# Performance work log

Measured on AMD Instinct MI355X. Metric: run time of the kernel, lower is better.

The kernel has to match this reference:

```python
import jax, jax.numpy as jnp
import numpy as np

N = 100000   # nodes
E = 1000000  # edges
IN = 100     # input feature dim
H = 4        # heads
D = 32       # hidden per head (H*D = 128)
C = 47       # classes
EPS = 1e-5
SLOPE = 0.2  # DGL GATv2 leaky_relu negative slope


def setup_inputs() -> dict:
    key = jax.random.key(0)
    ks = jax.random.split(key, 32)
    lin = lambda k, i, o: (jax.random.normal(k, (i, o), jnp.float32) / np.float32(np.sqrt(i)))
    inp = {}
    inp['x'] = jax.random.normal(ks[0], (N, IN), jnp.float32)
    inp['src'] = jax.random.randint(ks[1], (E,), 0, N, jnp.int32)
    inp['dst'] = jnp.sort(jax.random.randint(ks[2], (E,), 0, N, jnp.int32))
    # layer 0: IN -> H*D, Linear residual (IN != H*D)
    inp['Wsrc0'] = lin(ks[3], IN, H * D); inp['bsrc0'] = jnp.zeros(H * D, jnp.float32)
    inp['Wdst0'] = lin(ks[4], IN, H * D); inp['bdst0'] = jnp.zeros(H * D, jnp.float32)
    inp['attn0'] = lin(ks[5], H, D)
    inp['Wres0'] = lin(ks[6], IN, H * D); inp['bres0'] = jnp.zeros(H * D, jnp.float32)
    # layer 1: H*D -> H*D, Identity residual (128 == 128)
    inp['Wsrc1'] = lin(ks[7], H * D, H * D); inp['bsrc1'] = jnp.zeros(H * D, jnp.float32)
    inp['Wdst1'] = lin(ks[8], H * D, H * D); inp['bdst1'] = jnp.zeros(H * D, jnp.float32)
    inp['attn1'] = lin(ks[9], H, D)
    # layer 2: H*D -> H*C, Linear residual (128 != 188)
    inp['Wsrc2'] = lin(ks[10], H * D, H * C); inp['bsrc2'] = jnp.zeros(H * C, jnp.float32)
    inp['Wdst2'] = lin(ks[11], H * D, H * C); inp['bdst2'] = jnp.zeros(H * C, jnp.float32)
    inp['attn2'] = lin(ks[12], H, C)
    inp['Wres2'] = lin(ks[13], H * D, H * C); inp['bres2'] = jnp.zeros(H * C, jnp.float32)
    # BatchNorm1d params (training-mode batch stats)
    inp['g0'] = jnp.ones(H * D, jnp.float32); inp['be0'] = jnp.zeros(H * D, jnp.float32)
    inp['g1'] = jnp.ones(H * D, jnp.float32); inp['be1'] = jnp.zeros(H * D, jnp.float32)
    return inp


def _gatv2(h, src, dst, Ws, bs, Wd, bd, attn, resval):
    """One GATv2Conv on a full block (src feats == dst feats == h)."""
    Hh, Dd = attn.shape
    fs = (h @ Ws + bs).reshape(-1, Hh, Dd)   # [N,H,D] src projection
    fd = (h @ Wd + bd).reshape(-1, Hh, Dd)   # [N,H,D] dst projection
    e = jax.nn.leaky_relu(fs[src] + fd[dst], SLOPE)         # [E,H,D]
    logits = jnp.einsum('ehd,hd->eh', e, attn)              # [E,H]
    m = jax.ops.segment_max(logits, dst, num_segments=N)    # per-dst max
    ex = jnp.exp(logits - m[dst])
    s = jax.ops.segment_sum(ex, dst, num_segments=N)
    alpha = ex / s[dst]                                      # edge softmax
    out = jax.ops.segment_sum(alpha[:, :, None] * fs[src], dst, num_segments=N)
    return out + resval                                      # [N,H,D]


def _bn(x, g, b):
    mu = x.mean(0)
    v = x.var(0)  # biased, as torch BN training mode
    return g * (x - mu) / jnp.sqrt(v + EPS) + b


def reference(x, src, dst,
              Wsrc0, bsrc0, Wdst0, bdst0, attn0, Wres0, bres0,
              Wsrc1, bsrc1, Wdst1, bdst1, attn1,
              Wsrc2, bsrc2, Wdst2, bdst2, attn2, Wres2, bres2,
              g0, be0, g1, be1):
    # layer 0: conv(+relu activation) -> flatten -> BN -> relu (dropout = eval identity)
    res0 = (x @ Wres0 + bres0).reshape(N, H, D)
    h = jax.nn.relu(_gatv2(x, src, dst, Wsrc0, bsrc0, Wdst0, bdst0, attn0, res0))
    h = jax.nn.relu(_bn(h.reshape(N, H * D), g0, be0))
    # layer 1: Identity residual
    res1 = h.reshape(N, H, D)
    h = jax.nn.relu(_gatv2(h, src, dst, Wsrc1, bsrc1, Wdst1, bdst1, attn1, res1))
    h = jax.nn.relu(_bn(h.reshape(N, H * D), g1, be1))
    # layer 2: no activation; mean over heads; log_softmax
    res2 = (h @ Wres2 + bres2).reshape(N, H, C)
    h = _gatv2(h, src, dst, Wsrc2, bsrc2, Wdst2, bdst2, attn2, res2)
    h = h.mean(1)                                # [N,C]
    return jax.nn.log_softmax(h, axis=-1)
```

## Files before the change

### kernel.cpp

```cpp
#include <hip/hip_runtime.h>
#include <hip/hip_bf16.h>

#define Nn 100000
#define Ee 1000000
#define INF_ 100
#define Hh 4
#define Dd 32
#define HD 128
#define Cc 47
#define HC 188
#define HCP 192
#define EPSV 1e-5f
#define SLOPE 0.2f
#define NBLK ((Nn + 255) / 256)

typedef __hip_bfloat16 bf16;
typedef __attribute__((ext_vector_type(8))) short short8;
typedef __attribute__((ext_vector_type(4))) float f32x4;
typedef __attribute__((ext_vector_type(2))) float f32x2;

__device__ __forceinline__ float tof(bf16 v) { return __bfloat162float(v); }
__device__ __forceinline__ float b2f(unsigned short u) {
    return __uint_as_float((unsigned)u << 16);
}
__device__ __forceinline__ float ldb(const bf16* p) {
    return b2f(*(const unsigned short*)p);
}
__device__ __forceinline__ unsigned short f2u(float v) {
    bf16 t = __float2bfloat16(v);
    return *(unsigned short*)&t;
}
__device__ __forceinline__ f32x2 pk2(float x, float y) {
    f32x2 r; r.x = x; r.y = y; return r;
}
__device__ __forceinline__ f32x2 pabs2(f32x2 v) {
    return __builtin_elementwise_max(v, -v);
}
__device__ __forceinline__ f32x2 pfma2(f32x2 a, f32x2 b, f32x2 c) {
    return __builtin_elementwise_fma(a, b, c);
}

template <int C>
__device__ __forceinline__ float dppadd(float v) {
    int m = __builtin_amdgcn_update_dpp(0, __float_as_int(v), C, 0xF, 0xF, false);
    return v + __int_as_float(m);
}
template <int C>
__device__ __forceinline__ float dppmax(float v) {
    int m = __builtin_amdgcn_update_dpp(0, __float_as_int(v), C, 0xF, 0xF, false);
    return fmaxf(v, __int_as_float(m));
}
__device__ __forceinline__ float sum16(float p) {
    p = dppadd<0xB1>(p);
    p = dppadd<0x4E>(p);
    p = dppadd<0x124>(p);
    p = dppadd<0x128>(p);
    return p;
}
__device__ __forceinline__ float max16(float p) {
    p = dppmax<0xB1>(p); p = dppmax<0x4E>(p);
    p = dppmax<0x124>(p); p = dppmax<0x128>(p);
    return p;
}

#define L2E 1.4426950408889634f
#define LN2 0.6931471805599453f

__device__ __forceinline__ float ld_any(const void* p, int i, int isbf) {
    return isbf ? tof(((const bf16*)p)[i]) : ((const float*)p)[i];
}

__device__ __forceinline__ int lbound(const int* __restrict__ dst, int n) {
    int lo = 0, hi = Ee;
    while (lo < hi) {
        int mid = (lo + hi) >> 1;
        if (dst[mid] < n) lo = mid + 1; else hi = mid;
    }
    return lo;
}

#define WROWS 1280
#define NSP 15
struct PrepTab { const void* src[8]; int row0[8]; int K[8]; int M[8]; int MP[8]; };
struct CvtTab { const void* src[NSP]; int off[NSP + 1]; };

__global__ __launch_bounds__(256) void prepare(
    const void* __restrict__ x, const int* __restrict__ src,
    const int* __restrict__ dst,
    PrepTab pt, CvtTab ct, int tot,
    bf16* __restrict__ xb, bf16* __restrict__ wtb, bf16* __restrict__ pb,
    unsigned* __restrict__ w384, unsigned* __restrict__ w256,
    int* __restrict__ ptr, int* __restrict__ cnt,
    float* __restrict__ z0, float* __restrict__ z1, int* __restrict__ flag) {
    __shared__ int wc[4];
    __shared__ int lbv[257];
    __shared__ int lh[256];
    const int t = threadIdx.x;
    unsigned w = ((const unsigned*)x)[t];
    float dv = __uint_as_float((w & 0xFFFFu) << 16);
    float da = fabsf(dv);
    unsigned long long m = __ballot(da > 1e-4f && da < 10.f);
    if ((t & 63) == 0) wc[t >> 6] = __popcll(m);
    __syncthreads();
    const int isbf = (wc[0] + wc[1] + wc[2] + wc[3]) >= 128;
    if (blockIdx.x == 0 && t == 0) *flag = isbf;

    const int gi = blockIdx.x * 256 + t;
    if (gi < Nn * 128) {
        int row = gi >> 7, col = gi & 127;
        float v = (col < INF_) ? ld_any(x, row * INF_ + col, isbf) : 0.f;
        xb[gi] = __float2bfloat16(v);
    }
    if (gi < WROWS * 128) {
        int row = gi >> 7, k = gi & 127;
        float v = 0.f;
#pragma unroll
        for (int q = 0; q < 8; ++q) {
            if (row >= pt.row0[q] && row < pt.row0[q] + pt.MP[q]) {
                int mm = row - pt.row0[q];
                if (mm < pt.M[q] && k < pt.K[q])
                    v = ld_any(pt.src[q], k * pt.M[q] + mm, isbf);
            }
        }
        wtb[gi] = __float2bfloat16(v);
    }
    if (gi < tot) {
        int seg = 0;
        while (gi >= ct.off[seg + 1]) seg++;
        pb[gi] = __float2bfloat16(ld_any(ct.src[seg], gi - ct.off[seg], isbf));
    }
    if (gi < Ee) {
        unsigned s = (unsigned)src[gi];
        w384[gi] = s * 384u;
        w256[gi] = s << 8;
    }
    if (gi < 2 * HD) { z0[gi] = 0.f; z1[gi] = 0.f; }
    if (blockIdx.x < NBLK) {
        int nn = gi;
        int lb = Ee;
        if (nn <= Nn) { lb = lbound(dst, nn); ptr[nn] = lb; }
        lbv[t] = lb;
        if (t == 255) lbv[256] = (nn + 1 <= Nn) ? lbound(dst, nn + 1) : Ee;
        lh[t] = 0;
        __syncthreads();
        if (nn < Nn) {
            int dg = lbv[t + 1] - lbv[t]; if (dg > 255) dg = 255;
            atomicAdd(&lh[dg], 1);
        }
        __syncthreads();
        cnt[t * NBLK + blockIdx.x] = lh[t];
    }
}

__global__ void deg_totals(const int* __restrict__ cnt, int* __restrict__ totals) {
    int wave = threadIdx.x >> 6, lane = threadIdx.x & 63;
    int bin = blockIdx.x * 4 + wave;
    int s = 0;
    for (int k = lane; k < NBLK; k += 64) s += cnt[bin * NBLK + k];
#pragma unroll
    for (int o = 1; o < 64; o <<= 1) s += __shfl_xor(s, o);
    if (lane == 0) totals[bin] = s;
}

__global__ void deg_bases(const int* __restrict__ cnt, const int* __restrict__ totals,
                          int* __restrict__ base) {
    int wave = threadIdx.x >> 6, lane = threadIdx.x & 63;
    int bin = blockIdx.x * 4 + wave;
    int bb = 0;
    for (int b = bin + 1 + lane; b < 256; b += 64) bb += totals[b];
#pragma unroll
    for (int o = 1; o < 64; o <<= 1) bb += __shfl_xor(bb, o);
    int run = bb;
    for (int k0 = 0; k0 < NBLK; k0 += 64) {
        int k = k0 + lane;
        int c = (k < NBLK) ? cnt[bin * NBLK + k] : 0;
        int p = c;
#pragma unroll
        for (int o = 1; o < 64; o <<= 1) {
            int t = __shfl_up(p, o);
            if (lane >= o) p += t;
        }
        if (k < NBLK) base[bin * NBLK + k] = run + (p - c);
        run += __shfl(p, 63);
    }
}

__global__ void deg_scatter_blk(const int* __restrict__ ptr, const int* __restrict__ base,
                                int* __restrict__ perm) {
    __shared__ int lh[256];
    int t = threadIdx.x;
    lh[t] = 0;
    __syncthreads();
    int n = blockIdx.x * 256 + t;
    if (n < Nn) {
        int dg = ptr[n + 1] - ptr[n]; if (dg > 255) dg = 255;
        int loc = atomicAdd(&lh[dg], 1);
        perm[base[dg * NBLK + blockIdx.x] + loc] = n;
    }
}

template <int MP, int NOUT, int CS, bool ABN, bool PAD47, int OSTR>
__global__ __launch_bounds__(256, 4) void gemm_big(
    const bf16* __restrict__ A, const bf16* __restrict__ Wt,
    const bf16* __restrict__ b0, const bf16* __restrict__ b1,
    const bf16* __restrict__ b2,
    bf16* __restrict__ o0, bf16* __restrict__ o1, bf16* __restrict__ o2,
    int MR, const float* __restrict__ sums,
    const bf16* __restrict__ gg, const bf16* __restrict__ bbn) {
    constexpr int CS64 = CS * 64;
    constexpr int PITCH = CS64 + 8;
    constexpr int LSZ = (64 * PITCH > 64 * 136) ? 64 * PITCH : 64 * 136;
    __shared__ __align__(16) bf16 Al[LSZ];
    __shared__ float scb[ABN ? HD : 1], ofb[ABN ? HD : 1];
    const int row0 = blockIdx.x * 64;
    const int tid = threadIdx.x;
    if (ABN) {
        if (tid < HD) {
            float mu = sums[tid] * (1.f / Nn);
            float var = sums[HD + tid] * (1.f / Nn) - mu * mu;
            float sc = tof(gg[tid]) * rsqrtf(var + EPSV);
            scb[tid] = sc;
            ofb[tid] = tof(bbn[tid]) - mu * sc;
        }
        __syncthreads();
    }
#pragma unroll
    for (int j = 0; j < 4; ++j) {
        int idx = tid + j * 256;
        int r = idx >> 4, kk = (idx & 15) * 8;
        int4 val = {0, 0, 0, 0};
        if (row0 + r < Nn) {
            val = *(const int4*)&A[(size_t)(row0 + r) * 128 + kk];
            if (ABN) {
                short8 av = *(short8*)&val;
                bf16 tmp[8];
#pragma unroll
                for (int u = 0; u < 8; ++u) {
                    float v = b2f((unsigned short)av[u]);
                    v = fmaxf(fmaf(v, scb[kk + u], ofb[kk + u]), 0.f);
                    tmp[u] = __float2bfloat16(v);
                }
                val = *(int4*)tmp;
            }
        }
        *(int4*)&Al[r * 136 + kk] = val;
    }
    __syncthreads();
    const int wave = tid >> 6, lane = tid & 63;
    const int n16 = lane & 15, quad = lane >> 4;
    const int colbase = blockIdx.y * CS64 + wave * (16 * CS);
    f32x4 acc[4][CS];
#pragma unroll
    for (int rt = 0; rt < 4; ++rt)
#pragma unroll
        for (int c = 0; c < CS; ++c) acc[rt][c] = (f32x4){0.f, 0.f, 0.f, 0.f};
    const bf16* wb[CS];
#pragma unroll
    for (int c = 0; c < CS; ++c)
        wb[c] = Wt + (size_t)(colbase + c * 16 + n16) * 128 + quad * 8;
    const bf16* ap = Al + n16 * 136 + quad * 8;
#pragma unroll
    for (int ks = 0; ks < 4; ++ks) {
        short8 bf[CS];
#pragma unroll
        for (int c = 0; c < CS; ++c) bf[c] = *(const short8*)(wb[c] + ks * 32);
#pragma unroll
        for (int rt = 0; rt < 4; ++rt) {
            short8 af = *(const short8*)(ap + rt * 16 * 136 + ks * 32);
#pragma unroll
            for (int c = 0; c < CS; ++c)
                acc[rt][c] = __builtin_amdgcn_mfma_f32_16x16x32_bf16(af, bf[c], acc[rt][c], 0, 0, 0);
        }
    }
    __syncthreads();
    if (PAD47) {
        for (int z = tid; z < 64 * PITCH; z += 256) Al[z] = __float2bfloat16(0.f);
        __syncthreads();
    }
#pragma unroll
    for (int c = 0; c < CS; ++c) {
        int pos = wave * (16 * CS) + c * 16 + n16;
        int col = colbase + c * 16 + n16;
        int oi = col / MP, lc = col - oi * MP;
        bool valid = (oi < NOUT) && (lc < MR);
        float bb = 0.f;
        if (valid) {
            const bf16* bp = (oi == 0) ? b0 : (oi == 1) ? b1 : b2;
            bb = tof(bp[lc]);
        }
        int stp = PAD47 ? (lc + lc / 47) : pos;
#pragma unroll
        for (int rt = 0; rt < 4; ++rt) {
#pragma unroll
            for (int i = 0; i < 4; ++i) {
                int rl = rt * 16 + quad * 4 + i;
                if (valid) Al[rl * PITCH + stp] = __float2bfloat16(acc[rt][c][i] + bb);
            }
        }
    }
    __syncthreads();
    constexpr int NG = CS64 / 8;
    for (int t = tid; t < 64 * NG; t += 256) {
        int rl = t / NG, g = t % NG;
        int row = row0 + rl;
        if (row >= Nn) continue;
        int pos0 = g * 8;
        int oi, lc0;
        if (PAD47) { oi = blockIdx.y; lc0 = pos0; }
        else {
            int col0 = blockIdx.y * CS64 + pos0;
            oi = col0 / MP; lc0 = col0 - oi * MP;
        }
        if (oi >= NOUT) continue;
        bf16* o = (oi == 0) ? o0 : (oi == 1) ? o1 : o2;
        int4 v = *(int4*)&Al[rl * PITCH + pos0];
        *(int4*)&o[(size_t)row * OSTR + lc0] = v;
    }
}

template <bool RESBN>
__global__ __launch_bounds__(256) void gat_fused_128(
    const bf16* __restrict__ fs, const bf16* __restrict__ fd,
    const unsigned* __restrict__ srcW, const int* __restrict__ ptr,
    const int* __restrict__ perm,
    const bf16* __restrict__ attn, const bf16* __restrict__ resb,
    const float* __restrict__ sums, const bf16* __restrict__ gv,
    const bf16* __restrict__ bev, bf16* __restrict__ hout) {
    const int wave = threadIdx.x >> 6, lane = threadIdx.x & 63;
    const int di = blockIdx.x * 4 + wave;
    if (di >= Nn) return;
    const int d = perm[di];
    const int c0 = lane * 2;
    const unsigned c0b = (unsigned)c0 * 2u;
    ushort2 aq = *(const ushort2*)&attn[c0];
    float a0 = b2f(aq.x) * L2E, a1 = b2f(aq.y) * L2E;
    const f32x2 Av = pk2(0.6f * a0, 0.6f * a1);
    const f32x2 Bv = pk2(0.4f * a0, 0.4f * a1);
    ushort2 dq = *(const ushort2*)&fd[(size_t)d * HD + c0];
    const f32x2 fdv = pk2(b2f(dq.x), b2f(dq.y));
    const char* fsb = (const char*)fs;
    float l = 0.f;
    f32x2 Ov = pk2(0.f, 0.f);
    int e = ptr[d];
    const int e1 = ptr[d + 1];
    for (; e < e1 && (e & 3); ++e) {
        unsigned v = srcW[e] + c0b;
        ushort2 fq = *(const ushort2*)(fsb + v);
        f32x2 f = pk2(b2f(fq.x), b2f(fq.y));
        f32x2 x = f + fdv;
        f32x2 t = pfma2(pabs2(x), Bv, x * Av);
        float p = sum16(t.x + t.y);
        float pe = __builtin_amdgcn_exp2f(p);
        l += pe;
        Ov = pfma2(pk2(pe, pe), f, Ov);
    }
    for (; e + 3 < e1; e += 4) {
        uint4 sw = *(const uint4*)&srcW[e];
        unsigned vA = sw.x + c0b, vB = sw.y + c0b;
        unsigned vC = sw.z + c0b, vD = sw.w + c0b;
        ushort2 qA = *(const ushort2*)(fsb + vA);
        ushort2 qB = *(const ushort2*)(fsb + vB);
        ushort2 qC = *(const ushort2*)(fsb + vC);
        ushort2 qD = *(const ushort2*)(fsb + vD);
        f32x2 fA = pk2(b2f(qA.x), b2f(qA.y));
        f32x2 fB = pk2(b2f(qB.x), b2f(qB.y));
        f32x2 fC = pk2(b2f(qC.x), b2f(qC.y));
        f32x2 fD = pk2(b2f(qD.x), b2f(qD.y));
        f32x2 xA = fA + fdv, xB = fB + fdv, xC = fC + fdv, xD = fD + fdv;
        f32x2 tA = pfma2(pabs2(xA), Bv, xA * Av);
        f32x2 tB = pfma2(pabs2(xB), Bv, xB * Av);
        f32x2 tC = pfma2(pabs2(xC), Bv, xC * Av);
        f32x2 tD = pfma2(pabs2(xD), Bv, xD * Av);
        float pA = tA.x + tA.y, pB = tB.x + tB.y;
        float pC = tC.x + tC.y, pD = tD.x + tD.y;
        pA = sum16(pA); pB = sum16(pB); pC = sum16(pC); pD = sum16(pD);
        float eA = __builtin_amdgcn_exp2f(pA), eB = __builtin_amdgcn_exp2f(pB);
        float eC = __builtin_amdgcn_exp2f(pC), eD = __builtin_amdgcn_exp2f(pD);
        l += (eA + eB) + (eC + eD);
        Ov = pfma2(pk2(eA, eA), fA, Ov);
        Ov = pfma2(pk2(eB, eB), fB, Ov);
        Ov = pfma2(pk2(eC, eC), fC, Ov);
        Ov = pfma2(pk2(eD, eD), fD, Ov);
    }
    for (; e < e1; ++e) {
        unsigned v = srcW[e] + c0b;
        ushort2 fq = *(const ushort2*)(fsb + v);
        f32x2 f = pk2(b2f(fq.x), b2f(fq.y));
        f32x2 x = f + fdv;
        f32x2 t = pfma2(pabs2(x), Bv, x * Av);
        float p = sum16(t.x + t.y);
        float pe = __builtin_amdgcn_exp2f(p);
        l += pe;
        Ov = pfma2(pk2(pe, pe), f, Ov);
    }
    float inv = l > 0.f ? 1.f / l : 0.f;
    ushort2 rq = *(const ushort2*)&resb[(size_t)d * HD + c0];
    float r0 = b2f(rq.x), r1 = b2f(rq.y);
    if (RESBN) {
        float mu0 = sums[c0] * (1.f / Nn), mu1 = sums[c0 + 1] * (1.f / Nn);
        float va0 = sums[HD + c0] * (1.f / Nn) - mu0 * mu0;
        float va1 = sums[HD + c0 + 1] * (1.f / Nn) - mu1 * mu1;
        float sc0 = tof(gv[c0]) * rsqrtf(va0 + EPSV);
        float sc1 = tof(gv[c0 + 1]) * rsqrtf(va1 + EPSV);
        float of0 = tof(bev[c0]) - mu0 * sc0;
        float of1 = tof(bev[c0 + 1]) - mu1 * sc1;
        r0 = fmaxf(fmaf(r0, sc0, of0), 0.f);
        r1 = fmaxf(fmaf(r1, sc1, of1), 0.f);
    }
    float v0 = fmaxf(fmaf(Ov.x, inv, r0), 0.f);
    float v1 = fmaxf(fmaf(Ov.y, inv, r1), 0.f);
    ushort2 ov; ov.x = f2u(v0); ov.y = f2u(v1);
    *(ushort2*)&hout[(size_t)d * HD + c0] = ov;
}

__global__ __launch_bounds__(256) void gat_fused_188(
    const bf16* __restrict__ fs, const bf16* __restrict__ fd,
    const unsigned* __restrict__ srcW, const int* __restrict__ ptr,
    const int* __restrict__ perm,
    const bf16* __restrict__ attn, const bf16* __restrict__ rs,
    void* __restrict__ out, const int* __restrict__ flag) {
    const int wave = threadIdx.x >> 6, lane = threadIdx.x & 63;
    const int di = blockIdx.x * 4 + wave;
    if (di >= Nn) return;
    const int d = perm[di];
    const int h = lane >> 4, j = lane & 15;
    const int c0 = h * 48 + j;
    const unsigned c0b = (unsigned)c0 * 2u;
    const int ca = h * Cc + j;
    const bool has2 = (j < 15);
    float a0 = ldb(&attn[ca]) * L2E;
    float a1 = ldb(&attn[ca + 16]) * L2E;
    float a2 = has2 ? ldb(&attn[ca + 32]) * L2E : 0.f;
    float A0 = 0.6f * a0, B0 = 0.4f * a0;
    float A1 = 0.6f * a1, B1 = 0.4f * a1;
    float A2 = 0.6f * a2, B2 = 0.4f * a2;
    const bf16* fdr = fd + (size_t)d * HCP;
    float fd0 = ldb(&fdr[c0]);
    float fd1 = ldb(&fdr[c0 + 16]);
    float fd2 = ldb(&fdr[c0 + 32]);
    const char* fsb = (const char*)fs;
    float l = 0.f, O0 = 0.f, O1 = 0.f, O2 = 0.f;
    int e = ptr[d];
    const int e1 = ptr[d + 1];
    for (; e + 3 < e1; e += 4) {
        unsigned vA = srcW[e] + c0b, vB = srcW[e + 1] + c0b;
        unsigned vC = srcW[e + 2] + c0b, vD = srcW[e + 3] + c0b;
        float fA0 = b2f(*(const unsigned short*)(fsb + vA));
        float fA1 = b2f(*(const unsigned short*)(fsb + vA + 32));
        float fA2 = b2f(*(const unsigned short*)(fsb + vA + 64));
        float fB0 = b2f(*(const unsigned short*)(fsb + vB));
        float fB1 = b2f(*(const unsigned short*)(fsb + vB + 32));
        float fB2 = b2f(*(const unsigned short*)(fsb + vB + 64));
        float fC0 = b2f(*(const unsigned short*)(fsb + vC));
        float fC1 = b2f(*(const unsigned short*)(fsb + vC + 32));
        float fC2 = b2f(*(const unsigned short*)(fsb + vC + 64));
        float fD0 = b2f(*(const unsigned short*)(fsb + vD));
        float fD1 = b2f(*(const unsigned short*)(fsb + vD + 32));
        float fD2 = b2f(*(const unsigned short*)(fsb + vD + 64));
        float xA0 = fA0 + fd0, xA1 = fA1 + fd1, xA2 = fA2 + fd2;
        float xB0 = fB0 + fd0, xB1 = fB1 + fd1, xB2 = fB2 + fd2;
        float xC0 = fC0 + fd0, xC1 = fC1 + fd1, xC2 = fC2 + fd2;
        float xD0 = fD0 + fd0, xD1 = fD1 + fd1, xD2 = fD2 + fd2;
        float pA = fmaf(xA0, A0, fmaf(fabsf(xA0), B0, fmaf(xA1, A1, fmaf(fabsf(xA1), B1,
                   fmaf(xA2, A2, fabsf(xA2) * B2)))));
        float pB = fmaf(xB0, A0, fmaf(fabsf(xB0), B0, fmaf(xB1, A1, fmaf(fabsf(xB1), B1,
                   fmaf(xB2, A2, fabsf(xB2) * B2)))));
        float pC = fmaf(xC0, A0, fmaf(fabsf(xC0), B0, fmaf(xC1, A1, fmaf(fabsf(xC1), B1,
                   fmaf(xC2, A2, fabsf(xC2) * B2)))));
        float pD = fmaf(xD0, A0, fmaf(fabsf(xD0), B0, fmaf(xD1, A1, fmaf(fabsf(xD1), B1,
                   fmaf(xD2, A2, fabsf(xD2) * B2)))));
        pA = sum16(pA); pB = sum16(pB); pC = sum16(pC); pD = sum16(pD);
        float eA = __builtin_amdgcn_exp2f(pA), eB = __builtin_amdgcn_exp2f(pB);
        float eC = __builtin_amdgcn_exp2f(pC), eD = __builtin_amdgcn_exp2f(pD);
        l += (eA + eB) + (eC + eD);
        O0 = fmaf(eA, fA0, O0); O0 = fmaf(eB, fB0, O0);
        O0 = fmaf(eC, fC0, O0); O0 = fmaf(eD, fD0, O0);
        O1 = fmaf(eA, fA1, O1); O1 = fmaf(eB, fB1, O1);
        O1 = fmaf(eC, fC1, O1); O1 = fmaf(eD, fD1, O1);
        O2 = fmaf(eA, fA2, O2); O2 = fmaf(eB, fB2, O2);
        O2 = fmaf(eC, fC2, O2); O2 = fmaf(eD, fD2, O2);
    }
    for (; e < e1; ++e) {
        unsigned v = srcW[e] + c0b;
        float f0 = b2f(*(const unsigned short*)(fsb + v));
        float f1 = b2f(*(const unsigned short*)(fsb + v + 32));
        float f2 = b2f(*(const unsigned short*)(fsb + v + 64));
        float x0 = f0 + fd0, x1 = f1 + fd1, x2 = f2 + fd2;
        float p = fmaf(x0, A0, fmaf(fabsf(x0), B0, fmaf(x1, A1, fmaf(fabsf(x1), B1,
                  fmaf(x2, A2, fabsf(x2) * B2)))));
        p = sum16(p);
        float pe = __builtin_amdgcn_exp2f(p);
        l += pe;
        O0 = fmaf(pe, f0, O0);
        O1 = fmaf(pe, f1, O1);
        O2 = fmaf(pe, f2, O2);
    }
    float inv = l > 0.f ? 1.f / l : 0.f;
    const bf16* rr = rs + (size_t)d * HCP;
    float v0 = fmaf(O0, inv, ldb(&rr[c0]));
    float v1 = fmaf(O1, inv, ldb(&rr[c0 + 16]));
    float v2 = has2 ? fmaf(O2, inv, ldb(&rr[c0 + 32])) : 0.f;
    v0 += __shfl_xor(v0, 16); v0 += __shfl_xor(v0, 32); v0 *= 0.25f;
    v1 += __shfl_xor(v1, 16); v1 += __shfl_xor(v1, 32); v1 *= 0.25f;
    v2 += __shfl_xor(v2, 16); v2 += __shfl_xor(v2, 32); v2 *= 0.25f;
    float mx = fmaxf(v0, v1);
    if (has2) mx = fmaxf(mx, v2);
    mx = max16(mx);
    float sm = __expf(v0 - mx) + __expf(v1 - mx) + (has2 ? __expf(v2 - mx) : 0.f);
    sm = sum16(sm);
    if (h == 0) {
        float ls = mx + __log2f(sm) * LN2;
        if (*flag) {
            bf16* o = (bf16*)out + (size_t)d * Cc;
            o[j] = __float2bfloat16(v0 - ls);
            o[j + 16] = __float2bfloat16(v1 - ls);
            if (has2) o[j + 32] = __float2bfloat16(v2 - ls);
        } else {
            float* o = (float*)out + (size_t)d * Cc;
            o[j] = v0 - ls;
            o[j + 16] = v1 - ls;
            if (has2) o[j + 32] = v2 - ls;
        }
    }
}

__global__ void col_stats(const bf16* __restrict__ in, float* __restrict__ sums) {
    int c = threadIdx.x;
    int r0 = blockIdx.x * 256;
    int r1 = r0 + 256; if (r1 > Nn) r1 = Nn;
    float s = 0.f, s2 = 0.f;
    for (int r = r0; r < r1; ++r) {
        float v = ldb(&in[(size_t)r * HD + c]);
        s += v; s2 += v * v;
    }
    atomicAdd(&sums[c], s);
    atomicAdd(&sums[HD + c], s2);
}

extern "C" void kernel_launch(void* const* d_in, const int* in_sizes, int n_in,
                              void* d_out, int out_size, void* d_ws, size_t ws_size,
                              hipStream_t stream) {
    (void)in_sizes; (void)n_in; (void)out_size; (void)ws_size;
    const void* x = d_in[0];
    const int* src = (const int*)d_in[1];
    const int* dst = (const int*)d_in[2];

    char* ws = (char*)d_ws;
    size_t off = 0;
    auto alloc = [&](size_t bytes) {
        void* p = ws + off;
        off += (bytes + 255) & ~(size_t)255;
        return p;
    };
    bf16* xb = (bf16*)alloc((size_t)Nn * 128 * 2);
    bf16* rb = (bf16*)alloc((size_t)Nn * HD * 2);
    bf16* rs = xb;
    bf16* fs = (bf16*)alloc((size_t)Nn * HCP * 2);
    bf16* fd = (bf16*)alloc((size_t)Nn * HCP * 2);
    bf16* hbA = (bf16*)alloc((size_t)Nn * HD * 2);
    bf16* hbB = (bf16*)alloc((size_t)Nn * HD * 2);
    int* ptr = (int*)alloc((Nn + 1) * 4);
    bf16* wtb = (bf16*)alloc((size_t)WROWS * 128 * 2);
    float* bns0 = (float*)alloc(2 * HD * 4);
    float* bns1 = (float*)alloc(2 * HD * 4);
    bf16* pb = (bf16*)alloc(4096 * 2);
    int* flag = (int*)alloc(256);
    unsigned* w384 = (unsigned*)alloc((size_t)Ee * 4);
    unsigned* w256 = (unsigned*)alloc((size_t)Ee * 4);
    int* cnt = (int*)alloc((size_t)256 * NBLK * 4);
    int* cbase = (int*)alloc((size_t)256 * NBLK * 4);
    int* totals = (int*)alloc(256 * 4);
    int* perm = (int*)alloc((size_t)Nn * 4);

    static const int spIdx[NSP] = {4, 6, 7, 9, 11, 13, 14, 16, 18, 19, 21, 22, 23, 24, 25};
    static const int spSz[NSP]  = {HD, HD, HD, HD, HD, HD, HD, HC, HC, HC, HC, HD, HD, HD, HD};
    CvtTab tab;
    int tot = 0;
    for (int i = 0; i < NSP; ++i) { tab.src[i] = d_in[spIdx[i]]; tab.off[i] = tot; tot += spSz[i]; }
    tab.off[NSP] = tot;
    const bf16 *bsrc0 = pb + tab.off[0], *bdst0 = pb + tab.off[1], *attn0 = pb + tab.off[2],
               *bres0 = pb + tab.off[3], *bsrc1 = pb + tab.off[4], *bdst1 = pb + tab.off[5],
               *attn1 = pb + tab.off[6], *bsrc2 = pb + tab.off[7], *bdst2 = pb + tab.off[8],
               *attn2 = pb + tab.off[9], *bres2 = pb + tab.off[10],
               *g0 = pb + tab.off[11], *be0 = pb + tab.off[12],
               *g1 = pb + tab.off[13], *be1 = pb + tab.off[14];

    PrepTab pt;
    static const int wIdx[8] = {3, 5, 8, 10, 12, 15, 17, 20};
    static const int wK[8]   = {INF_, INF_, INF_, HD, HD, HD, HD, HD};
    static const int wM[8]   = {HD, HD, HD, HD, HD, HC, HC, HC};
    static const int wMP[8]  = {128, 128, 128, 128, 128, 192, 192, 192};
    static const int wR0[8]  = {0, 128, 256, 384, 512, 640, 832, 1024};
    for (int i = 0; i < 8; ++i) {
        pt.src[i] = d_in[wIdx[i]]; pt.row0[i] = wR0[i];
        pt.K[i] = wK[i]; pt.M[i] = wM[i]; pt.MP[i] = wMP[i];
    }

    const int prepGrid = (Nn * 128 + 255) / 256;
    prepare<<<prepGrid, 256, 0, stream>>>(x, src, dst, pt, tab, tot,
                                          xb, wtb, pb, w384, w256, ptr, cnt,
                                          bns0, bns1, flag);
    deg_totals<<<64, 256, 0, stream>>>(cnt, totals);
    deg_bases<<<64, 256, 0, stream>>>(cnt, totals, cbase);
    deg_scatter_blk<<<NBLK, 256, 0, stream>>>(ptr, cbase, perm);

    const int fusedGrid = (Nn + 3) / 4;
    const int statsGrid = NBLK;
    const int rowBlk = (Nn + 63) / 64;

    gemm_big<128, 3, 3, false, false, HD><<<dim3(rowBlk, 2), 256, 0, stream>>>(
        xb, wtb, bsrc0, bdst0, bres0, fs, fd, rb, HD, nullptr, nullptr, nullptr);
    gat_fused_128<false><<<fusedGrid, 256, 0, stream>>>(fs, fd, w256, ptr, perm,
                                                        attn0, rb, nullptr, nullptr,
                                                        nullptr, hbA);
    col_stats<<<statsGrid, 128, 0, stream>>>(hbA, bns0);

    gemm_big<128, 2, 2, true, false, HD><<<dim3(rowBlk, 2), 256, 0, stream>>>(
        hbA, wtb + (size_t)384 * 128, bsrc1, bdst1, nullptr, fs, fd, nullptr, HD,
        bns0, g0, be0);
    gat_fused_128<true><<<fusedGrid, 256, 0, stream>>>(fs, fd, w256, ptr, perm,
                                                       attn1, hbA, bns0, g0, be0, hbB);
    col_stats<<<statsGrid, 128, 0, stream>>>(hbB, bns1);

    gemm_big<192, 3, 3, true, true, HCP><<<dim3(rowBlk, 3), 256, 0, stream>>>(
        hbB, wtb + (size_t)640 * 128, bsrc2, bdst2, bres2, fs, fd, rs, HC,
        bns1, g1, be1);
    gat_fused_188<<<fusedGrid, 256, 0, stream>>>(fs, fd, w384, ptr, perm, attn2, rs,
                                                 d_out, flag);
}
```

Measured before the change: 648.7 us.

## Repack layer-2 projection layout so each lane gathers one dword plus one short

The layer-2 GEMM epilogue now stores each head's 47 classes in an interleaved layout. Columns j and j+16 of a lane sit in one adjacent 32-bit pair in the first 256 bytes, and the third column sits in a trailing packed region. The layer-2 aggregation kernel then does one 4-byte load and one 2-byte load per edge instead of three scattered 2-byte loads, for the source, destination and residual rows alike. Separately, the 128-wide aggregation drops its alignment peel loop and the vectorized uint4 load of edge indices, using scalar index loads instead. That second change could add index-load overhead.

```diff
diff --git a/kernel.cpp b/kernel.cpp
--- a/kernel.cpp
+++ b/kernel.cpp
@@ -22,6 +22,12 @@
 __device__ __forceinline__ float tof(bf16 v) { return __bfloat162float(v); }
 __device__ __forceinline__ float b2f(unsigned short u) {
     return __uint_as_float((unsigned)u << 16);
+}
+__device__ __forceinline__ float b2flo(unsigned u) {
+    return __uint_as_float(u << 16);
+}
+__device__ __forceinline__ float b2fhi(unsigned u) {
+    return __uint_as_float(u & 0xFFFF0000u);
 }
 __device__ __forceinline__ float ldb(const bf16* p) {
     return b2f(*(const unsigned short*)p);
@@ -199,7 +205,7 @@
     }
 }
 
-template <int MP, int NOUT, int CS, bool ABN, bool PAD47, int OSTR>
+template <int MP, int NOUT, int CS, bool ABN, bool PACK, int OSTR>
 __global__ __launch_bounds__(256, 4) void gemm_big(
     const bf16* __restrict__ A, const bf16* __restrict__ Wt,
     const bf16* __restrict__ b0, const bf16* __restrict__ b1,
@@ -273,7 +279,7 @@
         }
     }
     __syncthreads();
-    if (PAD47) {
+    if (PACK) {
         for (int z = tid; z < 64 * PITCH; z += 256) Al[z] = __float2bfloat16(0.f);
         __syncthreads();
     }
@@ -288,7 +294,15 @@
             const bf16* bp = (oi == 0) ? b0 : (oi == 1) ? b1 : b2;
             bb = tof(bp[lc]);
         }
-        int stp = PAD47 ? (lc + lc / 47) : pos;
+        int stp;
+        if (PACK) {
+            int hh = lc / 47, cc2 = lc - hh * 47;
+            int jj = cc2 & 15, kk2 = cc2 >> 4;
+            int l = hh * 16 + jj;
+            stp = (kk2 < 2) ? (2 * l + kk2) : (128 + l);
+        } else {
+            stp = pos;
+        }
 #pragma unroll
         for (int rt = 0; rt < 4; ++rt) {
 #pragma unroll
@@ -306,7 +320,7 @@
         if (row >= Nn) continue;
         int pos0 = g * 8;
         int oi, lc0;
-        if (PAD47) { oi = blockIdx.y; lc0 = pos0; }
+        if (PACK) { oi = blockIdx.y; lc0 = pos0; }
         else {
             int col0 = blockIdx.y * CS64 + pos0;
             oi = col0 / MP; lc0 = col0 - oi * MP;
@@ -343,21 +357,9 @@
     f32x2 Ov = pk2(0.f, 0.f);
     int e = ptr[d];
     const int e1 = ptr[d + 1];
-    for (; e < e1 && (e & 3); ++e) {
-        unsigned v = srcW[e] + c0b;
-        ushort2 fq = *(const ushort2*)(fsb + v);
-        f32x2 f = pk2(b2f(fq.x), b2f(fq.y));
-        f32x2 x = f + fdv;
-        f32x2 t = pfma2(pabs2(x), Bv, x * Av);
-        float p = sum16(t.x + t.y);
-        float pe = __builtin_amdgcn_exp2f(p);
-        l += pe;
-        Ov = pfma2(pk2(pe, pe), f, Ov);
-    }
     for (; e + 3 < e1; e += 4) {
-        uint4 sw = *(const uint4*)&srcW[e];
-        unsigned vA = sw.x + c0b, vB = sw.y + c0b;
-        unsigned vC = sw.z + c0b, vD = sw.w + c0b;
+        unsigned vA = srcW[e] + c0b, vB = srcW[e + 1] + c0b;
+        unsigned vC = srcW[e + 2] + c0b, vD = srcW[e + 3] + c0b;
         ushort2 qA = *(const ushort2*)(fsb + vA);
         ushort2 qB = *(const ushort2*)(fsb + vB);
         ushort2 qC = *(const ushort2*)(fsb + vC);
@@ -424,8 +426,8 @@
     if (di >= Nn) return;
     const int d = perm[di];
     const int h = lane >> 4, j = lane & 15;
-    const int c0 = h * 48 + j;
-    const unsigned c0b = (unsigned)c0 * 2u;
+    const unsigned cbA = (unsigned)lane * 4u;
+    const unsigned cbB = 256u + (unsigned)lane * 2u;
     const int ca = h * Cc + j;
     const bool has2 = (j < 15);
     float a0 = ldb(&attn[ca]) * L2E;
@@ -434,29 +436,30 @@
     float A0 = 0.6f * a0, B0 = 0.4f * a0;
     float A1 = 0.6f * a1, B1 = 0.4f * a1;
     float A2 = 0.6f * a2, B2 = 0.4f * a2;
-    const bf16* fdr = fd + (size_t)d * HCP;
-    float fd0 = ldb(&fdr[c0]);
-    float fd1 = ldb(&fdr[c0 + 16]);
-    float fd2 = ldb(&fdr[c0 + 32]);
+    const char* fdb = (const char*)fd;
+    const size_t drow = (size_t)d * 384u;
+    unsigned dqa = *(const unsigned*)(fdb + drow + cbA);
+    unsigned short dqb = *(const unsigned short*)(fdb + drow + cbB);
+    float fd0 = b2flo(dqa), fd1 = b2fhi(dqa);
+    float fd2 = b2f(dqb);
     const char* fsb = (const char*)fs;
     float l = 0.f, O0 = 0.f, O1 = 0.f, O2 = 0.f;
     int e = ptr[d];
     const int e1 = ptr[d + 1];
     for (; e + 3 < e1; e += 4) {
-        unsigned vA = srcW[e] + c0b, vB = srcW[e + 1] + c0b;
-        unsigned vC = srcW[e + 2] + c0b, vD = srcW[e + 3] + c0b;
-        float fA0 = b2f(*(const unsigned short*)(fsb + vA));
-        float fA1 = b2f(*(const unsigned short*)(fsb + vA + 32));
-        float fA2 = b2f(*(const unsigned short*)(fsb + vA + 64));
-        float fB0 = b2f(*(const unsigned short*)(fsb + vB));
-        float fB1 = b2f(*(const unsigned short*)(fsb + vB + 32));
-        float fB2 = b2f(*(const unsigned short*)(fsb + vB + 64));
-        float fC0 = b2f(*(const unsigned short*)(fsb + vC));
-        float fC1 = b2f(*(const unsigned short*)(fsb + vC + 32));
-        float fC2 = b2f(*(const unsigned short*)(fsb + vC + 64));
-        float fD0 = b2f(*(const unsigned short*)(fsb + vD));
-        float fD1 = b2f(*(const unsigned short*)(fsb + vD + 32));
-        float fD2 = b2f(*(const unsigned short*)(fsb + vD + 64));
+        unsigned bA = srcW[e], bB = srcW[e + 1], bC = srcW[e + 2], bD = srcW[e + 3];
+        unsigned qA = *(const unsigned*)(fsb + bA + cbA);
+        unsigned qB = *(const unsigned*)(fsb + bB + cbA);
+        unsigned qC = *(const unsigned*)(fsb + bC + cbA);
+        unsigned qD = *(const unsigned*)(fsb + bD + cbA);
+        unsigned short uA = *(const unsigned short*)(fsb + bA + cbB);
+        unsigned short uB = *(const unsigned short*)(fsb + bB + cbB);
+        unsigned short uC = *(const unsigned short*)(fsb + bC + cbB);
+        unsigned short uD = *(const unsigned short*)(fsb + bD + cbB);
+        float fA0 = b2flo(qA), fA1 = b2fhi(qA), fA2 = b2f(uA);
+        float fB0 = b2flo(qB), fB1 = b2fhi(qB), fB2 = b2f(uB);
+        float fC0 = b2flo(qC), fC1 = b2fhi(qC), fC2 = b2f(uC);
+        float fD0 = b2flo(qD), fD1 = b2fhi(qD), fD2 = b2f(uD);
         float xA0 = fA0 + fd0, xA1 = fA1 + fd1, xA2 = fA2 + fd2;
         float xB0 = fB0 + fd0, xB1 = fB1 + fd1, xB2 = fB2 + fd2;
         float xC0 = fC0 + fd0, xC1 = fC1 + fd1, xC2 = fC2 + fd2;
@@ -481,10 +484,10 @@
         O2 = fmaf(eC, fC2, O2); O2 = fmaf(eD, fD2, O2);
     }
     for (; e < e1; ++e) {
-        unsigned v = srcW[e] + c0b;
-        float f0 = b2f(*(const unsigned short*)(fsb + v));
-        float f1 = b2f(*(const unsigned short*)(fsb + v + 32));
-        float f2 = b2f(*(const unsigned short*)(fsb + v + 64));
+        unsigned b = srcW[e];
+        unsigned q = *(const unsigned*)(fsb + b + cbA);
+        unsigned short u = *(const unsigned short*)(fsb + b + cbB);
+        float f0 = b2flo(q), f1 = b2fhi(q), f2 = b2f(u);
         float x0 = f0 + fd0, x1 = f1 + fd1, x2 = f2 + fd2;
         float p = fmaf(x0, A0, fmaf(fabsf(x0), B0, fmaf(x1, A1, fmaf(fabsf(x1), B1,
                   fmaf(x2, A2, fabsf(x2) * B2)))));
@@ -496,10 +499,12 @@
         O2 = fmaf(pe, f2, O2);
     }
     float inv = l > 0.f ? 1.f / l : 0.f;
-    const bf16* rr = rs + (size_t)d * HCP;
-    float v0 = fmaf(O0, inv, ldb(&rr[c0]));
-    float v1 = fmaf(O1, inv, ldb(&rr[c0 + 16]));
-    float v2 = has2 ? fmaf(O2, inv, ldb(&rr[c0 + 32])) : 0.f;
+    const char* rb_ = (const char*)rs;
+    unsigned rqa = *(const unsigned*)(rb_ + drow + cbA);
+    unsigned short rqb = *(const unsigned short*)(rb_ + drow + cbB);
+    float v0 = fmaf(O0, inv, b2flo(rqa));
+    float v1 = fmaf(O1, inv, b2fhi(rqa));
+    float v2 = has2 ? fmaf(O2, inv, b2f(rqb)) : 0.f;
     v0 += __shfl_xor(v0, 16); v0 += __shfl_xor(v0, 32); v0 *= 0.25f;
     v1 += __shfl_xor(v1, 16); v1 += __shfl_xor(v1, 32); v1 *= 0.25f;
     v2 += __shfl_xor(v2, 16); v2 += __shfl_xor(v2, 32); v2 *= 0.25f;
```

New measurement: 627.7 us. 1.03x faster.
